# Kernel tuning notes

Hardware: AMD Instinct MI355X
Metric: run time of the kernel (lower is better)

Reference implementation:

```python
import jax, jax.numpy as jnp
import numpy as np

D_MODEL = 1024
N_HEADS = 16
D_HEAD = D_MODEL // N_HEADS
MEM_SIZE = 256


def setup_inputs() -> dict:
    key = jax.random.key(0)
    k_x, k_q, k_o, k_mk, k_mv = jax.random.split(key, 5)
    B, T = 4, 4096
    x = jax.random.normal(k_x, (B, T, D_MODEL), dtype=jnp.float32)
    # xavier_uniform for square Linear weights: bound = sqrt(6/(fan_in+fan_out))
    bound = float(np.sqrt(6.0 / (D_MODEL + D_MODEL)))
    Wq = jax.random.uniform(k_q, (D_MODEL, D_MODEL), minval=-bound, maxval=bound, dtype=jnp.float32)
    Wo = jax.random.uniform(k_o, (D_MODEL, D_MODEL), minval=-bound, maxval=bound, dtype=jnp.float32)
    # kaiming_uniform(a=sqrt(5)) on (H,S,D): fan_in = S*D (last two dims), bound = sqrt(6/((1+a^2)*fan_in)) = 1/sqrt(fan_in)
    bk = float(1.0 / np.sqrt(MEM_SIZE * D_HEAD))
    M_k = jax.random.uniform(k_mk, (N_HEADS, MEM_SIZE, D_HEAD), minval=-bk, maxval=bk, dtype=jnp.float32)
    M_v = jax.random.uniform(k_mv, (N_HEADS, MEM_SIZE, D_HEAD), minval=-0.01, maxval=0.01, dtype=jnp.float32)
    return {"x": x, "Wq": Wq, "Wo": Wo, "M_k": M_k, "M_v": M_v}


def reference(x, Wq, Wo, M_k, M_v):
    B, T, _ = x.shape
    H, S, D = N_HEADS, MEM_SIZE, D_HEAD
    # Q projection (torch Linear: x @ W^T) -> (B, H, T, D)
    Q = (x @ Wq.T).reshape(B, T, H, D).transpose(0, 2, 1, 3)
    scale = D ** -0.5
    # (B, H, T, S) attention against shared external keys
    attn = jnp.einsum("bhtd,hsd->bhts", Q, M_k) * scale
    attn = jax.nn.softmax(attn, axis=-1)
    # double normalization: L1 over the token (T) axis
    attn = attn / (attn.sum(axis=-2, keepdims=True) + 1e-6)
    # dropout = 0.0 (inference): no-op
    out = jnp.einsum("bhts,hsd->bhtd", attn, M_v)
    out = out.transpose(0, 2, 1, 3).reshape(B, T, H * D)
    return out @ Wo.T
```

## Files before the change

### kernel.cpp

```cpp
#include <hip/hip_runtime.h>
#include <math.h>

constexpr int B_  = 4;
constexpr int T_  = 4096;
constexpr int DM_ = 1024;
constexpr int H_  = 16;
constexpr int S_  = 256;
constexpr int BT_ = B_ * T_;
constexpr int NT_ = T_ / 64;
constexpr size_t QELEMS = (size_t)BT_ * DM_;

typedef _Float16 v8h __attribute__((ext_vector_type(8)));
typedef _Float16 v4h __attribute__((ext_vector_type(4)));
typedef float    v4f __attribute__((ext_vector_type(4)));

__device__ _Float16 g_AH[QELEMS];
__device__ _Float16 g_QH[QELEMS];
__device__ _Float16 g_WqH[DM_ * DM_];
__device__ _Float16 g_WoH[DM_ * DM_];
__device__ _Float16 g_MkH[H_ * S_ * 64];
__device__ _Float16 g_MvT[H_ * 64 * S_];
__device__ _Float16 g_Mv2[(size_t)B_ * H_ * 64 * S_];
__device__ _Float16 g_P[(size_t)B_ * H_ * T_ * S_];
__device__ float    g_cpart[(size_t)B_ * H_ * NT_ * S_];

__global__ __launch_bounds__(256) void cvt_h(const float* __restrict__ src,
                                             _Float16* __restrict__ dst,
                                             float scale) {
  const size_t i = (size_t)blockIdx.x * 256 + threadIdx.x;
  const float4* s = (const float4*)src;
  float4 a = s[2 * i], b = s[2 * i + 1];
  v8h o;
  o[0] = (_Float16)(a.x * scale); o[1] = (_Float16)(a.y * scale);
  o[2] = (_Float16)(a.z * scale); o[3] = (_Float16)(a.w * scale);
  o[4] = (_Float16)(b.x * scale); o[5] = (_Float16)(b.y * scale);
  o[6] = (_Float16)(b.z * scale); o[7] = (_Float16)(b.w * scale);
  *(v8h*)&dst[8 * i] = o;
}

__global__ __launch_bounds__(256) void transpose_mv(const float* __restrict__ Mv) {
  const int idx = blockIdx.x * 256 + threadIdx.x;
  const int h = idx >> 14, rem = idx & 16383;
  const int s = rem >> 6, d = rem & 63;
  g_MvT[h * 16384 + d * 256 + s] = (_Float16)Mv[idx];
}

template <typename OUT_T>
__device__ __forceinline__ void gemm_body(const _Float16* __restrict__ Ah,
                                          const _Float16* __restrict__ Wh,
                                          OUT_T* __restrict__ C, float scale) {
  __shared__ __align__(16) _Float16 As[128 * 64];
  __shared__ __align__(16) _Float16 Bs[128 * 64];
  const int tid  = threadIdx.x;
  const int n0   = blockIdx.x * 128;
  const int m0   = blockIdx.y * 128;
  const int wid  = tid >> 6;
  const int wm   = wid & 1;
  const int wn   = wid >> 1;
  const int lane = tid & 63;
  const int l15  = lane & 15;
  const int quad = lane >> 4;

  const int lrow = lane >> 3;
  const int gc   = (lane & 7) ^ lrow;
  const _Float16* agp = Ah + (size_t)(m0 + wid * 32 + lrow) * 1024 + gc * 8;
  const _Float16* bgp = Wh + (size_t)(n0 + wid * 32 + lrow) * 1024 + gc * 8;
  _Float16* asl = As + wid * 2048;
  _Float16* bsl = Bs + wid * 2048;

  v4f acc[4][4] = {};

  for (int k0 = 0; k0 < 1024; k0 += 64) {
#pragma unroll
    for (int j = 0; j < 4; ++j) {
      __builtin_amdgcn_global_load_lds(
          (const __attribute__((address_space(1))) unsigned int*)(agp + (size_t)j * 8192 + k0),
          (__attribute__((address_space(3))) unsigned int*)(asl + j * 512),
          16, 0, 0);
      __builtin_amdgcn_global_load_lds(
          (const __attribute__((address_space(1))) unsigned int*)(bgp + (size_t)j * 8192 + k0),
          (__attribute__((address_space(3))) unsigned int*)(bsl + j * 512),
          16, 0, 0);
    }
    __syncthreads();
#pragma unroll
    for (int kk = 0; kk < 2; ++kk) {
      v8h af[4], bf[4];
      const int chx = (kk * 4 + quad) ^ (l15 & 7);
#pragma unroll
      for (int i = 0; i < 4; ++i)
        af[i] = *(const v8h*)&As[(wm * 64 + i * 16 + l15) * 64 + chx * 8];
#pragma unroll
      for (int j = 0; j < 4; ++j)
        bf[j] = *(const v8h*)&Bs[(wn * 64 + j * 16 + l15) * 64 + chx * 8];
#pragma unroll
      for (int i = 0; i < 4; ++i)
#pragma unroll
        for (int j = 0; j < 4; ++j)
          acc[i][j] = __builtin_amdgcn_mfma_f32_16x16x32_f16(af[i], bf[j], acc[i][j], 0, 0, 0);
    }
    __syncthreads();
  }
#pragma unroll
  for (int i = 0; i < 4; ++i) {
    const size_t mrow = (size_t)(m0 + wm * 64 + i * 16 + quad * 4);
#pragma unroll
    for (int j = 0; j < 4; ++j) {
      const int ncol = n0 + wn * 64 + j * 16 + l15;
#pragma unroll
      for (int r = 0; r < 4; ++r)
        C[(mrow + r) * 1024 + ncol] = (OUT_T)(acc[i][j][r] * scale);
    }
  }
}

__global__ __launch_bounds__(256) void gemm_q16(const _Float16* __restrict__ Wq) {
  gemm_body<_Float16>(g_AH, Wq, g_QH, 1.0f);
}
__global__ __launch_bounds__(256) void gemm_o(const _Float16* __restrict__ Wo,
                                              float* __restrict__ out) {
  gemm_body<float>(g_AH, Wo, out, 1.0f / 512.0f);
}

__global__ __launch_bounds__(256, 4) void attn_p1() {
  __shared__ __align__(16) _Float16 Psh[64][272];
  __shared__ float csum_sh[4][256];
  const int tid  = threadIdx.x;
  const int bh   = blockIdx.x;
  const int b    = bh >> 4, h = bh & 15;
  const int tile = blockIdx.y;
  const int t0   = tile * 64;
  const int wid  = tid >> 6;
  const int lane = tid & 63;
  const int l15  = lane & 15;
  const int quad = lane >> 4;
  char* MkS = (char*)&Psh[0][0];

  const _Float16* qrow = &g_QH[(size_t)(b * T_ + t0 + wid * 16 + l15) * 1024 + h * 64];
  v8h a0 = *(const v8h*)&qrow[quad * 8];
  v8h a1 = *(const v8h*)&qrow[32 + quad * 8];

  {
    const _Float16* mkrow = &g_MkH[h * (S_ * 64) + tid * 64];
#pragma unroll
    for (int c = 0; c < 8; ++c) {
      v8h v = *(const v8h*)&mkrow[c * 8];
      *(v8h*)(MkS + tid * 128 + ((c ^ (tid & 7)) << 4)) = v;
    }
  }
  __syncthreads();

  v4f acc[16] = {};
#pragma unroll
  for (int st = 0; st < 16; ++st) {
    const int row = st * 16 + l15;
    const int sw  = row & 7;
    v8h b0 = *(const v8h*)(MkS + row * 128 + ((quad ^ sw) << 4));
    v8h b1 = *(const v8h*)(MkS + row * 128 + (((4 + quad) ^ sw) << 4));
    acc[st] = __builtin_amdgcn_mfma_f32_16x16x32_f16(a0, b0, acc[st], 0, 0, 0);
    acc[st] = __builtin_amdgcn_mfma_f32_16x16x32_f16(a1, b1, acc[st], 0, 0, 0);
  }

#pragma unroll
  for (int r = 0; r < 4; ++r) {
    float ssum = 0.0f;
#pragma unroll
    for (int st = 0; st < 16; ++st) {
      float p = __expf(acc[st][r]);
      acc[st][r] = p; ssum += p;
    }
    ssum += __shfl_xor(ssum, 1); ssum += __shfl_xor(ssum, 2);
    ssum += __shfl_xor(ssum, 4); ssum += __shfl_xor(ssum, 8);
    const float inv = 1.0f / ssum;
#pragma unroll
    for (int st = 0; st < 16; ++st) acc[st][r] *= inv;
  }

#pragma unroll
  for (int st = 0; st < 16; ++st) {
    float c = acc[st][0] + acc[st][1] + acc[st][2] + acc[st][3];
    c += __shfl_xor(c, 16);
    c += __shfl_xor(c, 32);
    if (quad == 0) csum_sh[wid][st * 16 + l15] = c;
  }
  __syncthreads();
  g_cpart[((size_t)bh * NT_ + tile) * 256 + tid] =
      csum_sh[0][tid] + csum_sh[1][tid] + csum_sh[2][tid] + csum_sh[3][tid];

#pragma unroll
  for (int st = 0; st < 16; ++st)
#pragma unroll
    for (int r = 0; r < 4; ++r)
      Psh[wid * 16 + quad * 4 + r][st * 16 + l15] = (_Float16)acc[st][r];
  __syncthreads();
  {
    const int rr = tid >> 2, q = tid & 3;
    _Float16* prow = &g_P[((size_t)bh * T_ + t0 + rr) * 256 + q * 64];
#pragma unroll
    for (int j = 0; j < 8; ++j)
      *(v8h*)&prow[j * 8] = *(const v8h*)&Psh[rr][q * 64 + j * 8];
  }
}

__global__ __launch_bounds__(256) void finish_scale_mv() {
  __shared__ float cs[256];
  const int bh = blockIdx.x;
  const int h  = bh & 15;
  const int s  = threadIdx.x;
  float acc = 0.0f;
#pragma unroll 8
  for (int k = 0; k < NT_; ++k)
    acc += g_cpart[((size_t)bh * NT_ + k) * 256 + s];
  cs[s] = 1.0f / (acc + 1e-6f);
  __syncthreads();
#pragma unroll
  for (int t = 0; t < 8; ++t) {
    const int idx = t * 256 + threadIdx.x;
    const int d  = idx >> 5;
    const int sc = (idx & 31) * 8;
    v8h mv = *(const v8h*)&g_MvT[(h * 64 + d) * 256 + sc];
    v8h o;
#pragma unroll
    for (int j = 0; j < 8; ++j) o[j] = (_Float16)((float)mv[j] * cs[sc + j]);
    *(v8h*)&g_Mv2[(size_t)bh * 16384 + d * 256 + sc] = o;
  }
}

__global__ __launch_bounds__(256, 2) void pv2() {
  const int tid  = threadIdx.x;
  const int bh   = blockIdx.x;
  const int b    = bh >> 4, h = bh & 15;
  const int gblk = blockIdx.y;
  const int wid  = tid >> 6;
  const int lane = tid & 63;
  const int l15  = lane & 15;
  const int quad = lane >> 4;

  const _Float16* mv2 = &g_Mv2[(size_t)bh * 16384];
  v8h af[4][8];
#pragma unroll
  for (int nt = 0; nt < 4; ++nt)
#pragma unroll
    for (int kc = 0; kc < 8; ++kc)
      af[nt][kc] = *(const v8h*)&mv2[(nt * 16 + l15) * 256 + kc * 32 + quad * 8];

  const int t0w = gblk * 512 + wid * 128;
  const _Float16* pbase = &g_P[((size_t)bh * T_ + t0w) * 256];
  _Float16* obase = &g_AH[((size_t)(b * T_ + t0w)) * 1024 + h * 64];

  v8h bf[8];
#pragma unroll
  for (int kc = 0; kc < 8; ++kc)
    bf[kc] = *(const v8h*)&pbase[(size_t)l15 * 256 + kc * 32 + quad * 8];

  for (int g = 0; g < 8; ++g) {
    v8h nbf[8];
    if (g < 7) {
#pragma unroll
      for (int kc = 0; kc < 8; ++kc)
        nbf[kc] = *(const v8h*)&pbase[(size_t)((g + 1) * 16 + l15) * 256 + kc * 32 + quad * 8];
    }
    v4f acc[4] = {};
#pragma unroll
    for (int kc = 0; kc < 8; ++kc)
#pragma unroll
      for (int nt = 0; nt < 4; ++nt)
        acc[nt] = __builtin_amdgcn_mfma_f32_16x16x32_f16(af[nt][kc], bf[kc], acc[nt], 0, 0, 0);

    _Float16* orow = &obase[(size_t)(g * 16 + l15) * 1024 + quad * 4];
#pragma unroll
    for (int nt = 0; nt < 4; ++nt) {
      v4h o;
#pragma unroll
      for (int r = 0; r < 4; ++r) o[r] = (_Float16)(acc[nt][r] * 512.0f);
      *(v4h*)&orow[nt * 16] = o;
    }
    if (g < 7) {
#pragma unroll
      for (int kc = 0; kc < 8; ++kc) bf[kc] = nbf[kc];
    }
  }
}

extern "C" void kernel_launch(void* const* d_in, const int* in_sizes, int n_in,
                              void* d_out, int out_size, void* d_ws, size_t ws_size,
                              hipStream_t stream) {
  const float* x  = (const float*)d_in[0];
  const float* Wq = (const float*)d_in[1];
  const float* Wo = (const float*)d_in[2];
  const float* Mk = (const float*)d_in[3];
  const float* Mv = (const float*)d_in[4];
  float* out = (float*)d_out;

  _Float16 *AH, *WqH, *WoH, *MkH;
  (void)hipGetSymbolAddress((void**)&AH,  HIP_SYMBOL(g_AH));
  (void)hipGetSymbolAddress((void**)&WqH, HIP_SYMBOL(g_WqH));
  (void)hipGetSymbolAddress((void**)&WoH, HIP_SYMBOL(g_WoH));
  (void)hipGetSymbolAddress((void**)&MkH, HIP_SYMBOL(g_MkH));

  cvt_h<<<8192, 256, 0, stream>>>(x,  AH, 1.0f);
  cvt_h<<<512,  256, 0, stream>>>(Wq, WqH, 1.0f);
  cvt_h<<<512,  256, 0, stream>>>(Wo, WoH, 1.0f);
  cvt_h<<<128,  256, 0, stream>>>(Mk, MkH, 0.125f);
  transpose_mv<<<1024, 256, 0, stream>>>(Mv);
  gemm_q16<<<dim3(DM_ / 128, BT_ / 128), 256, 0, stream>>>(WqH);
  attn_p1<<<dim3(B_ * H_, NT_), 256, 0, stream>>>();
  finish_scale_mv<<<B_ * H_, 256, 0, stream>>>();
  pv2<<<dim3(B_ * H_, 8), 256, 0, stream>>>();
  gemm_o<<<dim3(DM_ / 128, BT_ / 128), 256, 0, stream>>>(WoH, out);
}
```

Before: 352.0 us.

## Fuse prep kernels, swizzle P staging, split column-sum finish across more blocks

Merges the five conversion and transpose launches into one prep kernel and drops the host symbol-address lookups. attn_p1 now writes per-wave column partials straight to global memory instead of reducing them in shared memory, and stages P through an XOR-swizzled unpadded buffer. Together these shrink shared memory and allow occupancy 5. finish_scale_mv is split four ways per (b,h) to expose more parallelism. This quadruples the partial-sum traffic and the number of reduction reads.

```diff
diff --git a/kernel.cpp b/kernel.cpp
--- a/kernel.cpp
+++ b/kernel.cpp
@@ -22,12 +22,11 @@
 __device__ _Float16 g_MvT[H_ * 64 * S_];
 __device__ _Float16 g_Mv2[(size_t)B_ * H_ * 64 * S_];
 __device__ _Float16 g_P[(size_t)B_ * H_ * T_ * S_];
-__device__ float    g_cpart[(size_t)B_ * H_ * NT_ * S_];
-
-__global__ __launch_bounds__(256) void cvt_h(const float* __restrict__ src,
-                                             _Float16* __restrict__ dst,
-                                             float scale) {
-  const size_t i = (size_t)blockIdx.x * 256 + threadIdx.x;
+__device__ float    g_cpart[(size_t)B_ * H_ * NT_ * 4 * S_];
+
+__device__ __forceinline__ void cvt8(const float* __restrict__ src,
+                                     _Float16* __restrict__ dst,
+                                     size_t i, float scale) {
   const float4* s = (const float4*)src;
   float4 a = s[2 * i], b = s[2 * i + 1];
   v8h o;
@@ -38,11 +37,27 @@
   *(v8h*)&dst[8 * i] = o;
 }
 
-__global__ __launch_bounds__(256) void transpose_mv(const float* __restrict__ Mv) {
-  const int idx = blockIdx.x * 256 + threadIdx.x;
-  const int h = idx >> 14, rem = idx & 16383;
-  const int s = rem >> 6, d = rem & 63;
-  g_MvT[h * 16384 + d * 256 + s] = (_Float16)Mv[idx];
+__global__ __launch_bounds__(256) void prep(const float* __restrict__ x,
+                                            const float* __restrict__ Wq,
+                                            const float* __restrict__ Wo,
+                                            const float* __restrict__ Mk,
+                                            const float* __restrict__ Mv) {
+  const int bid = blockIdx.x;
+  const int tid = threadIdx.x;
+  if (bid < 8192) {
+    cvt8(x, g_AH, (size_t)bid * 256 + tid, 1.0f);
+  } else if (bid < 8704) {
+    cvt8(Wq, g_WqH, (size_t)(bid - 8192) * 256 + tid, 1.0f);
+  } else if (bid < 9216) {
+    cvt8(Wo, g_WoH, (size_t)(bid - 8704) * 256 + tid, 1.0f);
+  } else if (bid < 9344) {
+    cvt8(Mk, g_MkH, (size_t)(bid - 9216) * 256 + tid, 0.125f);
+  } else {
+    const int idx = (bid - 9344) * 256 + tid;
+    const int h = idx >> 14, rem = idx & 16383;
+    const int s = rem >> 6, d = rem & 63;
+    g_MvT[h * 16384 + d * 256 + s] = (_Float16)Mv[idx];
+  }
 }
 
 template <typename OUT_T>
@@ -114,17 +129,15 @@
   }
 }
 
-__global__ __launch_bounds__(256) void gemm_q16(const _Float16* __restrict__ Wq) {
-  gemm_body<_Float16>(g_AH, Wq, g_QH, 1.0f);
-}
-__global__ __launch_bounds__(256) void gemm_o(const _Float16* __restrict__ Wo,
-                                              float* __restrict__ out) {
-  gemm_body<float>(g_AH, Wo, out, 1.0f / 512.0f);
-}
-
-__global__ __launch_bounds__(256, 4) void attn_p1() {
-  __shared__ __align__(16) _Float16 Psh[64][272];
-  __shared__ float csum_sh[4][256];
+__global__ __launch_bounds__(256) void gemm_q16() {
+  gemm_body<_Float16>(g_AH, g_WqH, g_QH, 1.0f);
+}
+__global__ __launch_bounds__(256) void gemm_o(float* __restrict__ out) {
+  gemm_body<float>(g_AH, g_WoH, out, 1.0f / 512.0f);
+}
+
+__global__ __launch_bounds__(256, 5) void attn_p1() {
+  __shared__ __align__(16) _Float16 Psh[64][256];
   const int tid  = threadIdx.x;
   const int bh   = blockIdx.x;
   const int b    = bh >> 4, h = bh & 15;
@@ -181,48 +194,61 @@
     float c = acc[st][0] + acc[st][1] + acc[st][2] + acc[st][3];
     c += __shfl_xor(c, 16);
     c += __shfl_xor(c, 32);
-    if (quad == 0) csum_sh[wid][st * 16 + l15] = c;
-  }
-  __syncthreads();
-  g_cpart[((size_t)bh * NT_ + tile) * 256 + tid] =
-      csum_sh[0][tid] + csum_sh[1][tid] + csum_sh[2][tid] + csum_sh[3][tid];
+    if (quad == 0)
+      g_cpart[(((size_t)bh * NT_ + tile) * 4 + wid) * 256 + st * 16 + l15] = c;
+  }
+
+  __syncthreads();
 
 #pragma unroll
   for (int st = 0; st < 16; ++st)
 #pragma unroll
-    for (int r = 0; r < 4; ++r)
-      Psh[wid * 16 + quad * 4 + r][st * 16 + l15] = (_Float16)acc[st][r];
+    for (int r = 0; r < 4; ++r) {
+      const int row = wid * 16 + quad * 4 + r;
+      *(_Float16*)(MkS + row * 512 + ((st * 32 + l15 * 2) ^ ((row & 7) << 4))) =
+          (_Float16)acc[st][r];
+    }
   __syncthreads();
   {
     const int rr = tid >> 2, q = tid & 3;
     _Float16* prow = &g_P[((size_t)bh * T_ + t0 + rr) * 256 + q * 64];
 #pragma unroll
-    for (int j = 0; j < 8; ++j)
-      *(v8h*)&prow[j * 8] = *(const v8h*)&Psh[rr][q * 64 + j * 8];
+    for (int j = 0; j < 8; ++j) {
+      v8h v = *(const v8h*)(MkS + rr * 512 + ((q * 128 + j * 16) ^ ((rr & 7) << 4)));
+      *(v8h*)&prow[j * 8] = v;
+    }
   }
 }
 
 __global__ __launch_bounds__(256) void finish_scale_mv() {
-  __shared__ float cs[256];
-  const int bh = blockIdx.x;
-  const int h  = bh & 15;
-  const int s  = threadIdx.x;
+  __shared__ float part[4][64];
+  __shared__ float cs[64];
+  const int bh  = blockIdx.x >> 2;
+  const int sq  = blockIdx.x & 3;
+  const int h   = bh & 15;
+  const int col = threadIdx.x & 63;
+  const int kg  = threadIdx.x >> 6;
   float acc = 0.0f;
-#pragma unroll 8
-  for (int k = 0; k < NT_; ++k)
-    acc += g_cpart[((size_t)bh * NT_ + k) * 256 + s];
-  cs[s] = 1.0f / (acc + 1e-6f);
-  __syncthreads();
-#pragma unroll
-  for (int t = 0; t < 8; ++t) {
-    const int idx = t * 256 + threadIdx.x;
-    const int d  = idx >> 5;
-    const int sc = (idx & 31) * 8;
-    v8h mv = *(const v8h*)&g_MvT[(h * 64 + d) * 256 + sc];
+  for (int t = kg * 16; t < kg * 16 + 16; ++t)
+#pragma unroll
+    for (int w = 0; w < 4; ++w)
+      acc += g_cpart[(((size_t)bh * NT_ + t) * 4 + w) * 256 + sq * 64 + col];
+  part[kg][col] = acc;
+  __syncthreads();
+  if (kg == 0)
+    cs[col] = 1.0f / (part[0][col] + part[1][col] + part[2][col] + part[3][col] + 1e-6f);
+  __syncthreads();
+  const int d   = threadIdx.x >> 2;
+  const int lc0 = (threadIdx.x & 3) * 16;
+#pragma unroll
+  for (int u = 0; u < 2; ++u) {
+    const int lc = lc0 + u * 8;
+    const int s  = sq * 64 + lc;
+    v8h mv = *(const v8h*)&g_MvT[(h * 64 + d) * 256 + s];
     v8h o;
 #pragma unroll
-    for (int j = 0; j < 8; ++j) o[j] = (_Float16)((float)mv[j] * cs[sc + j]);
-    *(v8h*)&g_Mv2[(size_t)bh * 16384 + d * 256 + sc] = o;
+    for (int j = 0; j < 8; ++j) o[j] = (_Float16)((float)mv[j] * cs[lc + j]);
+    *(v8h*)&g_Mv2[(size_t)bh * 16384 + d * 256 + s] = o;
   }
 }
 
@@ -292,20 +318,10 @@
   const float* Mv = (const float*)d_in[4];
   float* out = (float*)d_out;
 
-  _Float16 *AH, *WqH, *WoH, *MkH;
-  (void)hipGetSymbolAddress((void**)&AH,  HIP_SYMBOL(g_AH));
-  (void)hipGetSymbolAddress((void**)&WqH, HIP_SYMBOL(g_WqH));
-  (void)hipGetSymbolAddress((void**)&WoH, HIP_SYMBOL(g_WoH));
-  (void)hipGetSymbolAddress((void**)&MkH, HIP_SYMBOL(g_MkH));
-
-  cvt_h<<<8192, 256, 0, stream>>>(x,  AH, 1.0f);
-  cvt_h<<<512,  256, 0, stream>>>(Wq, WqH, 1.0f);
-  cvt_h<<<512,  256, 0, stream>>>(Wo, WoH, 1.0f);
-  cvt_h<<<128,  256, 0, stream>>>(Mk, MkH, 0.125f);
-  transpose_mv<<<1024, 256, 0, stream>>>(Mv);
-  gemm_q16<<<dim3(DM_ / 128, BT_ / 128), 256, 0, stream>>>(WqH);
+  prep<<<10368, 256, 0, stream>>>(x, Wq, Wo, Mk, Mv);
+  gemm_q16<<<dim3(DM_ / 128, BT_ / 128), 256, 0, stream>>>();
   attn_p1<<<dim3(B_ * H_, NT_), 256, 0, stream>>>();
-  finish_scale_mv<<<B_ * H_, 256, 0, stream>>>();
+  finish_scale_mv<<<B_ * H_ * 4, 256, 0, stream>>>();
   pv2<<<dim3(B_ * H_, 8), 256, 0, stream>>>();
-  gemm_o<<<dim3(DM_ / 128, BT_ / 128), 256, 0, stream>>>(WoH, out);
-}
+  gemm_o<<<dim3(DM_ / 128, BT_ / 128), 256, 0, stream>>>(out);
+}
```

New measurement: 346.0 us. No clear change (-1.7%).
